# Kernel optimization log

Hardware: AMD Instinct MI355X
Metric: run time of the kernel (lower is better)

## Reference

```python
import jax, jax.numpy as jnp
import numpy as np

NW, NT, ND = 100000, 10000, 50000
D = 128
E = {"ww": 200000, "wt": 100000, "wd": 150000, "td": 100000, "tt": 50000}


def setup_inputs() -> dict:
    key = jax.random.key(0)
    ks = iter(jax.random.split(key, 40))
    inp = {
        "h_word": jax.random.normal(next(ks), (NW, D), dtype=jnp.float32),
        "h_topic": jax.random.normal(next(ks), (NT, D), dtype=jnp.float32),
        "h_doc": jax.random.normal(next(ks), (ND, D), dtype=jnp.float32),
    }
    for et in ["ww", "wt", "wd", "td", "tt"]:
        inp[f"W_{et}"] = jax.random.normal(next(ks), (D, D), dtype=jnp.float32) * 0.05
        inp[f"b_{et}"] = jax.random.normal(next(ks), (D,), dtype=jnp.float32) * 0.05
    sizes = {"ww": (NW, NW), "wt": (NW, NT), "wd": (NW, ND), "td": (NT, ND), "tt": (NT, NT)}
    for et, (ns, nd) in sizes.items():
        inp[f"src_{et}"] = jax.random.randint(next(ks), (E[et],), 0, ns, dtype=jnp.int32)
        inp[f"dst_{et}"] = jax.random.randint(next(ks), (E[et],), 0, nd, dtype=jnp.int32)
        inp[f"ew_{et}"] = jax.random.uniform(next(ks), (E[et],), dtype=jnp.float32)
    return inp


def _linear(x, W, b):
    # torch nn.Linear: y = x @ W.T + b, W is [out, in]
    return x @ W.T + b


def _mean_agg(h_src, src, dst, ew, n_dst):
    # message m_e = h_src[src_e] * ew_e (u_mul_e), then per-dst mean (fn.mean)
    m = h_src[src] * ew[:, None]                               # [E, D]
    s = jax.ops.segment_sum(m, dst, num_segments=n_dst)        # [n_dst, D]
    cnt = jax.ops.segment_sum(jnp.ones_like(ew), dst, num_segments=n_dst)
    return s / jnp.maximum(cnt, 1.0)[:, None]


def reference(h_word, h_topic, h_doc,
              W_ww, b_ww, W_wt, b_wt, W_wd, b_wd, W_td, b_td, W_tt, b_tt,
              src_ww, dst_ww, ew_ww, src_wt, dst_wt, ew_wt,
              src_wd, dst_wd, ew_wd, src_td, dst_td, ew_td,
              src_tt, dst_tt, ew_tt):
    # DGL loop overwrites src node 'h' in-place -> linears COMPOSE per src type,
    # and messages (resolved at multi_update_all) use the final composed 'h'.
    hw = _linear(_linear(_linear(h_word, W_ww, b_ww), W_wt, b_wt), W_wd, b_wd)
    ht = _linear(_linear(h_topic, W_td, b_td), W_tt, b_tt)
    nw, nt, nd = h_word.shape[0], h_topic.shape[0], h_doc.shape[0]
    # cross-relation 'sum' of per-relation means
    out_word = _mean_agg(hw, src_ww, dst_ww, ew_ww, nw)
    out_topic = _mean_agg(hw, src_wt, dst_wt, ew_wt, nt) + _mean_agg(ht, src_tt, dst_tt, ew_tt, nt)
    out_doc = _mean_agg(hw, src_wd, dst_wd, ew_wd, nd) + _mean_agg(ht, src_td, dst_td, ew_td, nd)
    # relu + dropout (eval mode -> identity); concatenate node types for a single output
    return jnp.concatenate([
        jax.nn.relu(out_word), jax.nn.relu(out_topic), jax.nn.relu(out_doc)
    ], axis=0)
```

## Files before the change

kernel.cpp:

```cpp
#include <hip/hip_runtime.h>
#include <hip/hip_bf16.h>

#define DIM 128
#define NWORD 100000
#define NTOPIC 10000
#define NDOC 50000
#define NOUT (NWORD + NTOPIC + NDOC)

#define E_WW 200000
#define E_WT 100000
#define E_WD 150000
#define E_TD 100000
#define E_TT 50000
#define E_TOT 600000

#define B_WW 0
#define B_WT 100000
#define B_TT 110000
#define B_WD 120000
#define B_TD 170000
#define NSLOT 220000
#define NBLK_SCAN 215

#define NBW 512
#define NBT 64

typedef __attribute__((ext_vector_type(8))) short bf16x8;
typedef __attribute__((ext_vector_type(8))) unsigned short u16x8;
typedef __attribute__((ext_vector_type(4))) float f32x4;

__device__ __forceinline__ unsigned short f2bf(float f) {
    __hip_bfloat16 h = __float2bfloat16(f);
    return __builtin_bit_cast(unsigned short, h);
}
__device__ __forceinline__ float b2f(unsigned short u) {
    return __builtin_bit_cast(float, (unsigned)u << 16);
}

__global__ __launch_bounds__(128) void prep1(
    const float* __restrict__ W_ww, const float* __restrict__ b_ww,
    const float* __restrict__ W_wt, const float* __restrict__ b_wt,
    const float* __restrict__ W_wd, const float* __restrict__ b_wd,
    const float* __restrict__ W_td, const float* __restrict__ b_td,
    const float* __restrict__ W_tt, const float* __restrict__ b_tt,
    float* __restrict__ A, unsigned short* __restrict__ Wbf_t,
    float* __restrict__ tmpb, float* __restrict__ c_t, unsigned* __restrict__ cnt)
{
    int b = blockIdx.x, j = threadIdx.x;
    for (int i = b * 128 + j; i < NSLOT; i += gridDim.x * 128) cnt[i] = 0u;

    if (b < 128) {
        const float* wr = &W_wd[b * 128];
        float s0 = 0.f, s1 = 0.f, s2 = 0.f, s3 = 0.f;
        for (int m = 0; m < 128; m += 4) {
            s0 = fmaf(wr[m + 0], W_wt[(m + 0) * 128 + j], s0);
            s1 = fmaf(wr[m + 1], W_wt[(m + 1) * 128 + j], s1);
            s2 = fmaf(wr[m + 2], W_wt[(m + 2) * 128 + j], s2);
            s3 = fmaf(wr[m + 3], W_wt[(m + 3) * 128 + j], s3);
        }
        A[b * 128 + j] = (s0 + s1) + (s2 + s3);
    } else if (b < 256) {
        int k = b - 128;
        const float* wr = &W_tt[j * 128];
        float s0 = 0.f, s1 = 0.f, s2 = 0.f, s3 = 0.f;
        for (int m = 0; m < 128; m += 4) {
            s0 = fmaf(wr[m + 0], W_td[(m + 0) * 128 + k], s0);
            s1 = fmaf(wr[m + 1], W_td[(m + 1) * 128 + k], s1);
            s2 = fmaf(wr[m + 2], W_td[(m + 2) * 128 + k], s2);
            s3 = fmaf(wr[m + 3], W_td[(m + 3) * 128 + k], s3);
        }
        Wbf_t[j * 128 + k] = f2bf((s0 + s1) + (s2 + s3));
    } else if (b == 256) {
        float s = b_wt[j];
        for (int m = 0; m < 128; ++m) s = fmaf(W_wt[j * 128 + m], b_ww[m], s);
        tmpb[j] = s;
    } else {
        float s = b_tt[j];
        for (int m = 0; m < 128; ++m) s = fmaf(W_tt[j * 128 + m], b_td[m], s);
        c_t[j] = s;
    }
}

__global__ __launch_bounds__(256) void prep2(
    const float* __restrict__ W_ww, const float* __restrict__ W_wd,
    const float* __restrict__ b_wd, const float* __restrict__ A,
    const float* __restrict__ tmpb,
    unsigned short* __restrict__ Wbf_w, float* __restrict__ c_w,
    const int* __restrict__ dst_ww, const int* __restrict__ dst_wt,
    const int* __restrict__ dst_wd, const int* __restrict__ dst_td,
    const int* __restrict__ dst_tt,
    unsigned* __restrict__ cnt, unsigned* __restrict__ rank)
{
    int b = blockIdx.x, tid = threadIdx.x;
    if (b < 64) {
        int k = b * 2 + (tid >> 7), j = tid & 127;
        const float* ar = &A[j * 128];
        float s0 = 0.f, s1 = 0.f, s2 = 0.f, s3 = 0.f;
        for (int m = 0; m < 128; m += 4) {
            s0 = fmaf(ar[m + 0], W_ww[(m + 0) * 128 + k], s0);
            s1 = fmaf(ar[m + 1], W_ww[(m + 1) * 128 + k], s1);
            s2 = fmaf(ar[m + 2], W_ww[(m + 2) * 128 + k], s2);
            s3 = fmaf(ar[m + 3], W_ww[(m + 3) * 128 + k], s3);
        }
        Wbf_w[j * 128 + k] = f2bf((s0 + s1) + (s2 + s3));
    } else if (b == 64) {
        if (tid < 128) {
            float s = b_wd[tid];
            for (int m = 0; m < 128; ++m) s = fmaf(W_wd[tid * 128 + m], tmpb[m], s);
            c_w[tid] = s;
        }
    } else {
        int g = (b - 65) * 256 + tid;
        int slotidx;
        if (g < E_WW)                            slotidx = B_WW + dst_ww[g];
        else if (g < E_WW + E_WT)                slotidx = B_WT + dst_wt[g - E_WW];
        else if (g < E_WW + E_WT + E_WD)         slotidx = B_WD + dst_wd[g - E_WW - E_WT];
        else if (g < E_WW + E_WT + E_WD + E_TD)  slotidx = B_TD + dst_td[g - E_WW - E_WT - E_WD];
        else if (g < E_TOT)                      slotidx = B_TT + dst_tt[g - E_WW - E_WT - E_WD - E_TD];
        else return;
        rank[g] = atomicAdd(&cnt[slotidx], 1u);
    }
}

__global__ __launch_bounds__(256) void transform_mfma(
    const float* __restrict__ xw, const unsigned short* __restrict__ Wbf_w,
    const float* __restrict__ cw, unsigned short* __restrict__ yw, int ntw,
    const float* __restrict__ xt, const unsigned short* __restrict__ Wbf_t,
    const float* __restrict__ ct, unsigned short* __restrict__ yt, int ntt)
{
    __shared__ __attribute__((aligned(16))) unsigned short xs_all[4][16 * 128];
    const int tid = threadIdx.x;
    const int wid = tid >> 6, l = tid & 63;
    char* xs = (char*)xs_all[wid];
    const int l15 = l & 15, l4 = l >> 4;

    const bool isw = blockIdx.x < NBW;
    const float* x = isw ? xw : xt;
    const unsigned short* Wbf = isw ? Wbf_w : Wbf_t;
    const float* bias = isw ? cw : ct;
    unsigned short* y = isw ? yw : yt;
    const int nt = isw ? ntw : ntt;
    const int t0 = (isw ? blockIdx.x : blockIdx.x - NBW) * 4 + wid;
    const int tstr = (isw ? NBW : NBT) * 4;

    bf16x8 wf[8][4];
#pragma unroll
    for (int cg = 0; cg < 8; ++cg)
#pragma unroll
        for (int ki = 0; ki < 4; ++ki)
            wf[cg][ki] = *(const bf16x8*)&Wbf[(cg * 16 + l15) * 128 + ki * 32 + l4 * 8];

    float bj[8];
#pragma unroll
    for (int cg = 0; cg < 8; ++cg) bj[cg] = bias[cg * 16 + l15];

    const int row_s = l >> 2, ch = l & 3;

    float4 u[4], v[4];
    if (t0 < nt) {
        const float* xr = &x[((size_t)t0 * 16 + row_s) * 128 + ch * 32];
#pragma unroll
        for (int c = 0; c < 4; ++c) { u[c] = *(const float4*)(xr + c * 8); v[c] = *(const float4*)(xr + c * 8 + 4); }
    }

    for (int tile = t0; tile < nt; tile += tstr) {
#pragma unroll
        for (int c = 0; c < 4; ++c) {
            u16x8 p;
            p[0] = f2bf(u[c].x); p[1] = f2bf(u[c].y); p[2] = f2bf(u[c].z); p[3] = f2bf(u[c].w);
            p[4] = f2bf(v[c].x); p[5] = f2bf(v[c].y); p[6] = f2bf(v[c].z); p[7] = f2bf(v[c].w);
            int off = row_s * 256 + ((ch * 64 + c * 16) ^ ((row_s & 7) << 4));
            *(u16x8*)(xs + off) = p;
        }
        int nxt = tile + tstr;
        if (nxt < nt) {
            const float* xr = &x[((size_t)nxt * 16 + row_s) * 128 + ch * 32];
#pragma unroll
            for (int c = 0; c < 4; ++c) { u[c] = *(const float4*)(xr + c * 8); v[c] = *(const float4*)(xr + c * 8 + 4); }
        }

        f32x4 acc[8];
        const f32x4 zero = {0.f, 0.f, 0.f, 0.f};
#pragma unroll
        for (int cg = 0; cg < 8; ++cg) acc[cg] = zero;

#pragma unroll
        for (int ki = 0; ki < 4; ++ki) {
            int aoff = l15 * 256 + ((ki * 64 + l4 * 16) ^ ((l15 & 7) << 4));
            bf16x8 af = *(const bf16x8*)(xs + aoff);
#pragma unroll
            for (int cg = 0; cg < 8; ++cg)
                acc[cg] = __builtin_amdgcn_mfma_f32_16x16x32_bf16(af, wf[cg][ki], acc[cg], 0, 0, 0);
        }

        unsigned short* yr = &y[((size_t)tile * 16 + l4 * 4) * 128 + l15];
#pragma unroll
        for (int cg = 0; cg < 8; ++cg)
#pragma unroll
            for (int r = 0; r < 4; ++r)
                yr[r * 128 + cg * 16] = f2bf(acc[cg][r] + bj[cg]);
    }
}

__global__ __launch_bounds__(256) void scanA(const unsigned* __restrict__ cnt,
                                             unsigned* __restrict__ bsum)
{
    __shared__ unsigned sh[256];
    int t = threadIdx.x;
    int base = blockIdx.x * 1024 + t * 4;
    unsigned s = 0;
#pragma unroll
    for (int i = 0; i < 4; ++i) { int idx = base + i; if (idx < NSLOT) s += cnt[idx]; }
    sh[t] = s; __syncthreads();
    for (int o = 128; o > 0; o >>= 1) { if (t < o) sh[t] += sh[t + o]; __syncthreads(); }
    if (t == 0) bsum[blockIdx.x] = sh[0];
}

__global__ __launch_bounds__(256) void scanB(const unsigned* __restrict__ bsum,
                                             unsigned* __restrict__ boff)
{
    __shared__ unsigned sh[256];
    int t = threadIdx.x;
    unsigned v = (t < NBLK_SCAN) ? bsum[t] : 0u;
    sh[t] = v; __syncthreads();
    for (int o = 1; o < 256; o <<= 1) {
        unsigned x = (t >= o) ? sh[t - o] : 0u;
        __syncthreads();
        sh[t] += x;
        __syncthreads();
    }
    if (t < NBLK_SCAN) boff[t] = sh[t] - v;
}

__global__ __launch_bounds__(256) void scanC(const unsigned* __restrict__ cnt,
                                             const unsigned* __restrict__ boff,
                                             unsigned* __restrict__ offs)
{
    __shared__ unsigned sh[256];
    int t = threadIdx.x;
    int base = blockIdx.x * 1024 + t * 4;
    unsigned c[4]; unsigned s = 0;
#pragma unroll
    for (int i = 0; i < 4; ++i) {
        int idx = base + i;
        c[i] = (idx < NSLOT) ? cnt[idx] : 0u;
        s += c[i];
    }
    sh[t] = s; __syncthreads();
    for (int o = 1; o < 256; o <<= 1) {
        unsigned x = (t >= o) ? sh[t - o] : 0u;
        __syncthreads();
        sh[t] += x;
        __syncthreads();
    }
    unsigned run = boff[blockIdx.x] + sh[t] - s;
#pragma unroll
    for (int i = 0; i < 4; ++i) {
        int idx = base + i;
        if (idx < NSLOT) {
            offs[idx] = run;
            run += c[i];
            if (idx == NSLOT - 1) offs[NSLOT] = run;
        }
    }
}

__global__ void place(const int* __restrict__ dst_ww, const int* __restrict__ dst_wt,
                      const int* __restrict__ dst_wd, const int* __restrict__ dst_td,
                      const int* __restrict__ dst_tt,
                      const int* __restrict__ src_ww, const int* __restrict__ src_wt,
                      const int* __restrict__ src_wd, const int* __restrict__ src_td,
                      const int* __restrict__ src_tt,
                      const float* __restrict__ ew_ww, const float* __restrict__ ew_wt,
                      const float* __restrict__ ew_wd, const float* __restrict__ ew_td,
                      const float* __restrict__ ew_tt,
                      const unsigned* __restrict__ offs, const unsigned* __restrict__ rank,
                      uint2* __restrict__ se)
{
    int g = blockIdx.x * 256 + threadIdx.x;
    int slotidx, e; unsigned sv; float wv;
    if (g < E_WW)                            { e = g;                             slotidx = B_WW + dst_ww[e]; sv = src_ww[e]; wv = ew_ww[e]; }
    else if (g < E_WW + E_WT)                { e = g - E_WW;                      slotidx = B_WT + dst_wt[e]; sv = src_wt[e]; wv = ew_wt[e]; }
    else if (g < E_WW + E_WT + E_WD)         { e = g - E_WW - E_WT;               slotidx = B_WD + dst_wd[e]; sv = src_wd[e]; wv = ew_wd[e]; }
    else if (g < E_WW + E_WT + E_WD + E_TD)  { e = g - E_WW - E_WT - E_WD;        slotidx = B_TD + dst_td[e]; sv = src_td[e]; wv = ew_td[e]; }
    else if (g < E_TOT)                      { e = g - E_WW - E_WT - E_WD - E_TD; slotidx = B_TT + dst_tt[e]; sv = src_tt[e]; wv = ew_tt[e]; }
    else return;
    se[offs[slotidx] + rank[g]] = make_uint2(sv, __builtin_bit_cast(unsigned, wv));
}

__device__ __forceinline__ float4 seg_mean_bf(int slot,
                                              const unsigned* __restrict__ offs,
                                              const uint2* __restrict__ se,
                                              const unsigned short* __restrict__ h, int d4)
{
    unsigned off = offs[slot];
    unsigned deg = offs[slot + 1] - off;
    float ax = 0.f, ay = 0.f, az = 0.f, aw = 0.f;
    for (unsigned j = 0; j < deg; j += 4) {
        uint2 r0 = se[off + j];
        uint2 r1 = se[off + j + 1];
        uint2 r2 = se[off + j + 2];
        uint2 r3 = se[off + j + 3];
        unsigned s0 = r0.x;
        float    w0 = __builtin_bit_cast(float, r0.y);
        unsigned s1 = (j + 1 < deg) ? r1.x : 0u;
        float    w1 = (j + 1 < deg) ? __builtin_bit_cast(float, r1.y) : 0.f;
        unsigned s2 = (j + 2 < deg) ? r2.x : 0u;
        float    w2 = (j + 2 < deg) ? __builtin_bit_cast(float, r2.y) : 0.f;
        unsigned s3 = (j + 3 < deg) ? r3.x : 0u;
        float    w3 = (j + 3 < deg) ? __builtin_bit_cast(float, r3.y) : 0.f;
        ushort4 a0 = *(const ushort4*)&h[(size_t)s0 * 128 + d4];
        ushort4 a1 = *(const ushort4*)&h[(size_t)s1 * 128 + d4];
        ushort4 a2 = *(const ushort4*)&h[(size_t)s2 * 128 + d4];
        ushort4 a3 = *(const ushort4*)&h[(size_t)s3 * 128 + d4];
        ax = fmaf(b2f(a0.x), w0, ax); ay = fmaf(b2f(a0.y), w0, ay);
        az = fmaf(b2f(a0.z), w0, az); aw = fmaf(b2f(a0.w), w0, aw);
        ax = fmaf(b2f(a1.x), w1, ax); ay = fmaf(b2f(a1.y), w1, ay);
        az = fmaf(b2f(a1.z), w1, az); aw = fmaf(b2f(a1.w), w1, aw);
        ax = fmaf(b2f(a2.x), w2, ax); ay = fmaf(b2f(a2.y), w2, ay);
        az = fmaf(b2f(a2.z), w2, az); aw = fmaf(b2f(a2.w), w2, aw);
        ax = fmaf(b2f(a3.x), w3, ax); ay = fmaf(b2f(a3.y), w3, ay);
        az = fmaf(b2f(a3.z), w3, az); aw = fmaf(b2f(a3.w), w3, aw);
    }
    float inv = 1.0f / (float)(deg > 1u ? deg : 1u);
    return float4{ax * inv, ay * inv, az * inv, aw * inv};
}

__global__ void gather(const unsigned* __restrict__ offs,
                       const uint2* __restrict__ se,
                       const unsigned short* __restrict__ hw,
                       const unsigned short* __restrict__ ht,
                       float* __restrict__ out)
{
    int g = blockIdx.x * 256 + threadIdx.x;
    int n = g >> 5, d4 = (g & 31) << 2;
    if (n >= NOUT) return;
    float4 r;
    if (n < NWORD) {
        r = seg_mean_bf(B_WW + n, offs, se, hw, d4);
    } else if (n < NWORD + NTOPIC) {
        int i = n - NWORD;
        float4 a = seg_mean_bf(B_WT + i, offs, se, hw, d4);
        float4 b = seg_mean_bf(B_TT + i, offs, se, ht, d4);
        r = float4{a.x + b.x, a.y + b.y, a.z + b.z, a.w + b.w};
    } else {
        int i = n - NWORD - NTOPIC;
        float4 a = seg_mean_bf(B_WD + i, offs, se, hw, d4);
        float4 b = seg_mean_bf(B_TD + i, offs, se, ht, d4);
        r = float4{a.x + b.x, a.y + b.y, a.z + b.z, a.w + b.w};
    }
    r.x = fmaxf(r.x, 0.f); r.y = fmaxf(r.y, 0.f);
    r.z = fmaxf(r.z, 0.f); r.w = fmaxf(r.w, 0.f);
    *reinterpret_cast<float4*>(&out[(size_t)n * 128 + d4]) = r;
}

extern "C" void kernel_launch(void* const* d_in, const int* in_sizes, int n_in,
                              void* d_out, int out_size, void* d_ws, size_t ws_size,
                              hipStream_t stream) {
    const float* h_word  = (const float*)d_in[0];
    const float* h_topic = (const float*)d_in[1];
    const float* W_ww = (const float*)d_in[3];  const float* b_ww = (const float*)d_in[4];
    const float* W_wt = (const float*)d_in[5];  const float* b_wt = (const float*)d_in[6];
    const float* W_wd = (const float*)d_in[7];  const float* b_wd = (const float*)d_in[8];
    const float* W_td = (const float*)d_in[9];  const float* b_td = (const float*)d_in[10];
    const float* W_tt = (const float*)d_in[11]; const float* b_tt = (const float*)d_in[12];
    const int*   src_ww = (const int*)d_in[13]; const int* dst_ww = (const int*)d_in[14];
    const float* ew_ww  = (const float*)d_in[15];
    const int*   src_wt = (const int*)d_in[16]; const int* dst_wt = (const int*)d_in[17];
    const float* ew_wt  = (const float*)d_in[18];
    const int*   src_wd = (const int*)d_in[19]; const int* dst_wd = (const int*)d_in[20];
    const float* ew_wd  = (const float*)d_in[21];
    const int*   src_td = (const int*)d_in[22]; const int* dst_td = (const int*)d_in[23];
    const float* ew_td  = (const float*)d_in[24];
    const int*   src_tt = (const int*)d_in[25]; const int* dst_tt = (const int*)d_in[26];
    const float* ew_tt  = (const float*)d_in[27];

    float* out = (float*)d_out;

    unsigned short* hw_bf = (unsigned short*)d_ws;
    unsigned short* ht_bf = hw_bf + (size_t)NWORD * 128;
    unsigned short* Wbf_w = ht_bf + (size_t)NTOPIC * 128;
    unsigned short* Wbf_t = Wbf_w + 16384;
    float* fbase = (float*)(Wbf_t + 16384);
    float* c_w   = fbase;
    float* c_t   = c_w + 128;
    float* Amat  = c_t + 128;
    float* tmpb  = Amat + 16384;
    uint2* se    = (uint2*)(tmpb + 128);
    unsigned* cnt  = (unsigned*)(se + E_TOT + 4);
    unsigned* offs = cnt + NSLOT;
    unsigned* rank = offs + NSLOT + 1;
    unsigned* bsum = rank + E_TOT;
    unsigned* boff = bsum + 256;

    prep1<<<258, 128, 0, stream>>>(W_ww, b_ww, W_wt, b_wt, W_wd, b_wd, W_td, b_td,
                                   W_tt, b_tt, Amat, Wbf_t, tmpb, c_t, cnt);
    prep2<<<65 + (E_TOT + 255) / 256, 256, 0, stream>>>(
        W_ww, W_wd, b_wd, Amat, tmpb, Wbf_w, c_w,
        dst_ww, dst_wt, dst_wd, dst_td, dst_tt, cnt, rank);

    scanA<<<NBLK_SCAN, 256, 0, stream>>>(cnt, bsum);
    scanB<<<1, 256, 0, stream>>>(bsum, boff);
    scanC<<<NBLK_SCAN, 256, 0, stream>>>(cnt, boff, offs);
    place<<<(E_TOT + 255) / 256, 256, 0, stream>>>(
        dst_ww, dst_wt, dst_wd, dst_td, dst_tt,
        src_ww, src_wt, src_wd, src_td, src_tt,
        ew_ww, ew_wt, ew_wd, ew_td, ew_tt, offs, rank, se);

    transform_mfma<<<NBW + NBT, 256, 0, stream>>>(
        h_word,  Wbf_w, c_w, hw_bf, NWORD / 16,
        h_topic, Wbf_t, c_t, ht_bf, NTOPIC / 16);

    gather<<<(NOUT * 32 + 255) / 256, 256, 0, stream>>>(offs, se, hw_bf, ht_bf, out);
}
```

Measured before the change: 301.3 us.

## Fuse CSR build into one persistent kernel with grid barriers; split gather across half-waves

Merges prep2, the three scan kernels and the place kernel into a single persistent csr_build kernel. It uses 215 co-resident blocks that synchronise through atomic grid barriers, which removes four kernel launches and their inter-kernel gaps. The gather kernel now gives each output node 64 lanes: word nodes split their edge loop across two halves, and topic and doc nodes handle their two relations in parallel halves, combined with a cross-lane shuffle. This adds parallelism per node. The transform block counts also change. The grid barrier depends on all blocks being resident at once, which risks deadlock if occupancy assumptions fail.

Measured after the change: 347.6 us. 1.15x slower.

```diff
diff --git a/kernel.cpp b/kernel.cpp
--- a/kernel.cpp
+++ b/kernel.cpp
@@ -20,10 +20,11 @@
 #define B_WD 120000
 #define B_TD 170000
 #define NSLOT 220000
-#define NBLK_SCAN 215
-
-#define NBW 512
-#define NBT 64
+
+#define NBLK_CSR 215
+
+#define NBW 466
+#define NBT 46
 
 typedef __attribute__((ext_vector_type(8))) short bf16x8;
 typedef __attribute__((ext_vector_type(8))) unsigned short u16x8;
@@ -35,6 +36,24 @@
 }
 __device__ __forceinline__ float b2f(unsigned short u) {
     return __builtin_bit_cast(float, (unsigned)u << 16);
+}
+
+#define AGENT __HIP_MEMORY_SCOPE_AGENT
+__device__ __forceinline__ unsigned aload(const unsigned* p) {
+    return __hip_atomic_load(p, __ATOMIC_RELAXED, AGENT);
+}
+__device__ __forceinline__ void astore(unsigned* p, unsigned v) {
+    __hip_atomic_store(p, v, __ATOMIC_RELAXED, AGENT);
+}
+
+__device__ __forceinline__ void gbar(unsigned* bar, unsigned target) {
+    __syncthreads();
+    if (threadIdx.x == 0) {
+        __hip_atomic_fetch_add(bar, 1u, __ATOMIC_ACQ_REL, AGENT);
+        while (__hip_atomic_load(bar, __ATOMIC_ACQUIRE, AGENT) < target)
+            __builtin_amdgcn_s_sleep(4);
+    }
+    __syncthreads();
 }
 
 __global__ __launch_bounds__(128) void prep1(
@@ -44,10 +63,10 @@
     const float* __restrict__ W_td, const float* __restrict__ b_td,
     const float* __restrict__ W_tt, const float* __restrict__ b_tt,
     float* __restrict__ A, unsigned short* __restrict__ Wbf_t,
-    float* __restrict__ tmpb, float* __restrict__ c_t, unsigned* __restrict__ cnt)
+    float* __restrict__ tmpb, float* __restrict__ c_t, unsigned* __restrict__ zbase)
 {
     int b = blockIdx.x, j = threadIdx.x;
-    for (int i = b * 128 + j; i < NSLOT; i += gridDim.x * 128) cnt[i] = 0u;
+    for (int i = b * 128 + j; i < NSLOT + 16; i += gridDim.x * 128) zbase[i] = 0u;
 
     if (b < 128) {
         const float* wr = &W_wd[b * 128];
@@ -81,7 +100,18 @@
     }
 }
 
-__global__ __launch_bounds__(256) void prep2(
+__device__ __forceinline__ int edge_slot(
+    int g, const int* __restrict__ dw, const int* __restrict__ dt,
+    const int* __restrict__ dd, const int* __restrict__ dtd, const int* __restrict__ dtt)
+{
+    if (g < E_WW)                           return B_WW + dw[g];
+    if (g < E_WW + E_WT)                    return B_WT + dt[g - E_WW];
+    if (g < E_WW + E_WT + E_WD)             return B_WD + dd[g - E_WW - E_WT];
+    if (g < E_WW + E_WT + E_WD + E_TD)      return B_TD + dtd[g - E_WW - E_WT - E_WD];
+    return B_TT + dtt[g - E_WW - E_WT - E_WD - E_TD];
+}
+
+__global__ __launch_bounds__(256) void csr_build(
     const float* __restrict__ W_ww, const float* __restrict__ W_wd,
     const float* __restrict__ b_wd, const float* __restrict__ A,
     const float* __restrict__ tmpb,
@@ -89,11 +119,21 @@
     const int* __restrict__ dst_ww, const int* __restrict__ dst_wt,
     const int* __restrict__ dst_wd, const int* __restrict__ dst_td,
     const int* __restrict__ dst_tt,
-    unsigned* __restrict__ cnt, unsigned* __restrict__ rank)
-{
-    int b = blockIdx.x, tid = threadIdx.x;
+    const int* __restrict__ src_ww, const int* __restrict__ src_wt,
+    const int* __restrict__ src_wd, const int* __restrict__ src_td,
+    const int* __restrict__ src_tt,
+    const float* __restrict__ ew_ww, const float* __restrict__ ew_wt,
+    const float* __restrict__ ew_wd, const float* __restrict__ ew_td,
+    const float* __restrict__ ew_tt,
+    unsigned* __restrict__ cnt, unsigned* __restrict__ rank,
+    unsigned* __restrict__ offs, unsigned* __restrict__ bsum,
+    unsigned* __restrict__ bar, uint2* __restrict__ se)
+{
+    __shared__ unsigned sh[256];
+    const int b = blockIdx.x, t = threadIdx.x;
+
     if (b < 64) {
-        int k = b * 2 + (tid >> 7), j = tid & 127;
+        int k = b * 2 + (t >> 7), j = t & 127;
         const float* ar = &A[j * 128];
         float s0 = 0.f, s1 = 0.f, s2 = 0.f, s3 = 0.f;
         for (int m = 0; m < 128; m += 4) {
@@ -103,22 +143,57 @@
             s3 = fmaf(ar[m + 3], W_ww[(m + 3) * 128 + k], s3);
         }
         Wbf_w[j * 128 + k] = f2bf((s0 + s1) + (s2 + s3));
-    } else if (b == 64) {
-        if (tid < 128) {
-            float s = b_wd[tid];
-            for (int m = 0; m < 128; ++m) s = fmaf(W_wd[tid * 128 + m], tmpb[m], s);
-            c_w[tid] = s;
-        }
-    } else {
-        int g = (b - 65) * 256 + tid;
-        int slotidx;
-        if (g < E_WW)                            slotidx = B_WW + dst_ww[g];
-        else if (g < E_WW + E_WT)                slotidx = B_WT + dst_wt[g - E_WW];
-        else if (g < E_WW + E_WT + E_WD)         slotidx = B_WD + dst_wd[g - E_WW - E_WT];
-        else if (g < E_WW + E_WT + E_WD + E_TD)  slotidx = B_TD + dst_td[g - E_WW - E_WT - E_WD];
-        else if (g < E_TOT)                      slotidx = B_TT + dst_tt[g - E_WW - E_WT - E_WD - E_TD];
-        else return;
-        rank[g] = atomicAdd(&cnt[slotidx], 1u);
+    } else if (b == 64 && t < 128) {
+        float s = b_wd[t];
+        for (int m = 0; m < 128; ++m) s = fmaf(W_wd[t * 128 + m], tmpb[m], s);
+        c_w[t] = s;
+    }
+    for (int g = b * 256 + t; g < E_TOT; g += NBLK_CSR * 256) {
+        int slotidx = edge_slot(g, dst_ww, dst_wt, dst_wd, dst_td, dst_tt);
+        unsigned r = atomicAdd(&cnt[slotidx], 1u);
+        astore(&rank[g], r);
+    }
+    gbar(bar, NBLK_CSR);
+
+    const int base = b * 1024 + t * 4;
+    unsigned c0 = 0, c1 = 0, c2 = 0, c3 = 0;
+    if (base + 0 < NSLOT) c0 = aload(&cnt[base + 0]);
+    if (base + 1 < NSLOT) c1 = aload(&cnt[base + 1]);
+    if (base + 2 < NSLOT) c2 = aload(&cnt[base + 2]);
+    if (base + 3 < NSLOT) c3 = aload(&cnt[base + 3]);
+    unsigned s = c0 + c1 + c2 + c3;
+    sh[t] = s; __syncthreads();
+    for (int o = 1; o < 256; o <<= 1) {
+        unsigned x = (t >= o) ? sh[t - o] : 0u;
+        __syncthreads();
+        sh[t] += x;
+        __syncthreads();
+    }
+    const unsigned excl = sh[t] - s;
+    if (t == 0) astore(&bsum[b], sh[255]);
+    gbar(bar, 2 * NBLK_CSR);
+
+    unsigned p = (t < b) ? aload(&bsum[t]) : 0u;
+    sh[t] = p; __syncthreads();
+    for (int o = 128; o > 0; o >>= 1) { if (t < o) sh[t] += sh[t + o]; __syncthreads(); }
+    unsigned run = sh[0] + excl;
+    if (base + 0 < NSLOT) { astore(&offs[base + 0], run); run += c0; }
+    if (base + 1 < NSLOT) { astore(&offs[base + 1], run); run += c1; }
+    if (base + 2 < NSLOT) { astore(&offs[base + 2], run); run += c2; }
+    if (base + 3 < NSLOT) { astore(&offs[base + 3], run); run += c3; }
+    if (b == 0 && t == 0) astore(&offs[NSLOT], (unsigned)E_TOT);
+    gbar(bar, 3 * NBLK_CSR);
+
+    for (int g = b * 256 + t; g < E_TOT; g += NBLK_CSR * 256) {
+        int slotidx, e; unsigned sv; float wv;
+        if (g < E_WW)                           { e = g;                             slotidx = B_WW + dst_ww[e]; sv = src_ww[e]; wv = ew_ww[e]; }
+        else if (g < E_WW + E_WT)               { e = g - E_WW;                      slotidx = B_WT + dst_wt[e]; sv = src_wt[e]; wv = ew_wt[e]; }
+        else if (g < E_WW + E_WT + E_WD)        { e = g - E_WW - E_WT;               slotidx = B_WD + dst_wd[e]; sv = src_wd[e]; wv = ew_wd[e]; }
+        else if (g < E_WW + E_WT + E_WD + E_TD) { e = g - E_WW - E_WT - E_WD;        slotidx = B_TD + dst_td[e]; sv = src_td[e]; wv = ew_td[e]; }
+        else                                    { e = g - E_WW - E_WT - E_WD - E_TD; slotidx = B_TT + dst_tt[e]; sv = src_tt[e]; wv = ew_tt[e]; }
+        unsigned r = aload(&rank[g]);
+        unsigned o = aload(&offs[slotidx]);
+        se[o + r] = make_uint2(sv, __builtin_bit_cast(unsigned, wv));
     }
 }
 
@@ -202,113 +277,25 @@
     }
 }
 
-__global__ __launch_bounds__(256) void scanA(const unsigned* __restrict__ cnt,
-                                             unsigned* __restrict__ bsum)
-{
-    __shared__ unsigned sh[256];
-    int t = threadIdx.x;
-    int base = blockIdx.x * 1024 + t * 4;
-    unsigned s = 0;
-#pragma unroll
-    for (int i = 0; i < 4; ++i) { int idx = base + i; if (idx < NSLOT) s += cnt[idx]; }
-    sh[t] = s; __syncthreads();
-    for (int o = 128; o > 0; o >>= 1) { if (t < o) sh[t] += sh[t + o]; __syncthreads(); }
-    if (t == 0) bsum[blockIdx.x] = sh[0];
-}
-
-__global__ __launch_bounds__(256) void scanB(const unsigned* __restrict__ bsum,
-                                             unsigned* __restrict__ boff)
-{
-    __shared__ unsigned sh[256];
-    int t = threadIdx.x;
-    unsigned v = (t < NBLK_SCAN) ? bsum[t] : 0u;
-    sh[t] = v; __syncthreads();
-    for (int o = 1; o < 256; o <<= 1) {
-        unsigned x = (t >= o) ? sh[t - o] : 0u;
-        __syncthreads();
-        sh[t] += x;
-        __syncthreads();
-    }
-    if (t < NBLK_SCAN) boff[t] = sh[t] - v;
-}
-
-__global__ __launch_bounds__(256) void scanC(const unsigned* __restrict__ cnt,
-                                             const unsigned* __restrict__ boff,
-                                             unsigned* __restrict__ offs)
-{
-    __shared__ unsigned sh[256];
-    int t = threadIdx.x;
-    int base = blockIdx.x * 1024 + t * 4;
-    unsigned c[4]; unsigned s = 0;
-#pragma unroll
-    for (int i = 0; i < 4; ++i) {
-        int idx = base + i;
-        c[i] = (idx < NSLOT) ? cnt[idx] : 0u;
-        s += c[i];
-    }
-    sh[t] = s; __syncthreads();
-    for (int o = 1; o < 256; o <<= 1) {
-        unsigned x = (t >= o) ? sh[t - o] : 0u;
-        __syncthreads();
-        sh[t] += x;
-        __syncthreads();
-    }
-    unsigned run = boff[blockIdx.x] + sh[t] - s;
-#pragma unroll
-    for (int i = 0; i < 4; ++i) {
-        int idx = base + i;
-        if (idx < NSLOT) {
-            offs[idx] = run;
-            run += c[i];
-            if (idx == NSLOT - 1) offs[NSLOT] = run;
-        }
-    }
-}
-
-__global__ void place(const int* __restrict__ dst_ww, const int* __restrict__ dst_wt,
-                      const int* __restrict__ dst_wd, const int* __restrict__ dst_td,
-                      const int* __restrict__ dst_tt,
-                      const int* __restrict__ src_ww, const int* __restrict__ src_wt,
-                      const int* __restrict__ src_wd, const int* __restrict__ src_td,
-                      const int* __restrict__ src_tt,
-                      const float* __restrict__ ew_ww, const float* __restrict__ ew_wt,
-                      const float* __restrict__ ew_wd, const float* __restrict__ ew_td,
-                      const float* __restrict__ ew_tt,
-                      const unsigned* __restrict__ offs, const unsigned* __restrict__ rank,
-                      uint2* __restrict__ se)
-{
-    int g = blockIdx.x * 256 + threadIdx.x;
-    int slotidx, e; unsigned sv; float wv;
-    if (g < E_WW)                            { e = g;                             slotidx = B_WW + dst_ww[e]; sv = src_ww[e]; wv = ew_ww[e]; }
-    else if (g < E_WW + E_WT)                { e = g - E_WW;                      slotidx = B_WT + dst_wt[e]; sv = src_wt[e]; wv = ew_wt[e]; }
-    else if (g < E_WW + E_WT + E_WD)         { e = g - E_WW - E_WT;               slotidx = B_WD + dst_wd[e]; sv = src_wd[e]; wv = ew_wd[e]; }
-    else if (g < E_WW + E_WT + E_WD + E_TD)  { e = g - E_WW - E_WT - E_WD;        slotidx = B_TD + dst_td[e]; sv = src_td[e]; wv = ew_td[e]; }
-    else if (g < E_TOT)                      { e = g - E_WW - E_WT - E_WD - E_TD; slotidx = B_TT + dst_tt[e]; sv = src_tt[e]; wv = ew_tt[e]; }
-    else return;
-    se[offs[slotidx] + rank[g]] = make_uint2(sv, __builtin_bit_cast(unsigned, wv));
-}
-
-__device__ __forceinline__ float4 seg_mean_bf(int slot,
-                                              const unsigned* __restrict__ offs,
-                                              const uint2* __restrict__ se,
-                                              const unsigned short* __restrict__ h, int d4)
-{
-    unsigned off = offs[slot];
-    unsigned deg = offs[slot + 1] - off;
+__device__ __forceinline__ float4 seg_sum4(unsigned off, unsigned deg, unsigned j0,
+                                           unsigned step,
+                                           const uint2* __restrict__ se,
+                                           const unsigned short* __restrict__ h, int d4)
+{
     float ax = 0.f, ay = 0.f, az = 0.f, aw = 0.f;
-    for (unsigned j = 0; j < deg; j += 4) {
+    for (unsigned j = j0; j < deg; j += 4 * step) {
         uint2 r0 = se[off + j];
-        uint2 r1 = se[off + j + 1];
-        uint2 r2 = se[off + j + 2];
-        uint2 r3 = se[off + j + 3];
+        uint2 r1 = se[off + j + step];
+        uint2 r2 = se[off + j + 2 * step];
+        uint2 r3 = se[off + j + 3 * step];
         unsigned s0 = r0.x;
         float    w0 = __builtin_bit_cast(float, r0.y);
-        unsigned s1 = (j + 1 < deg) ? r1.x : 0u;
-        float    w1 = (j + 1 < deg) ? __builtin_bit_cast(float, r1.y) : 0.f;
-        unsigned s2 = (j + 2 < deg) ? r2.x : 0u;
-        float    w2 = (j + 2 < deg) ? __builtin_bit_cast(float, r2.y) : 0.f;
-        unsigned s3 = (j + 3 < deg) ? r3.x : 0u;
-        float    w3 = (j + 3 < deg) ? __builtin_bit_cast(float, r3.y) : 0.f;
+        unsigned s1 = (j + step < deg) ? r1.x : 0u;
+        float    w1 = (j + step < deg) ? __builtin_bit_cast(float, r1.y) : 0.f;
+        unsigned s2 = (j + 2 * step < deg) ? r2.x : 0u;
+        float    w2 = (j + 2 * step < deg) ? __builtin_bit_cast(float, r2.y) : 0.f;
+        unsigned s3 = (j + 3 * step < deg) ? r3.x : 0u;
+        float    w3 = (j + 3 * step < deg) ? __builtin_bit_cast(float, r3.y) : 0.f;
         ushort4 a0 = *(const ushort4*)&h[(size_t)s0 * 128 + d4];
         ushort4 a1 = *(const ushort4*)&h[(size_t)s1 * 128 + d4];
         ushort4 a2 = *(const ushort4*)&h[(size_t)s2 * 128 + d4];
@@ -322,36 +309,51 @@
         ax = fmaf(b2f(a3.x), w3, ax); ay = fmaf(b2f(a3.y), w3, ay);
         az = fmaf(b2f(a3.z), w3, az); aw = fmaf(b2f(a3.w), w3, aw);
     }
-    float inv = 1.0f / (float)(deg > 1u ? deg : 1u);
-    return float4{ax * inv, ay * inv, az * inv, aw * inv};
-}
-
-__global__ void gather(const unsigned* __restrict__ offs,
-                       const uint2* __restrict__ se,
-                       const unsigned short* __restrict__ hw,
-                       const unsigned short* __restrict__ ht,
-                       float* __restrict__ out)
+    return float4{ax, ay, az, aw};
+}
+
+__global__ __launch_bounds__(256) void gather(
+    const unsigned* __restrict__ offs, const uint2* __restrict__ se,
+    const unsigned short* __restrict__ hw, const unsigned short* __restrict__ ht,
+    float* __restrict__ out)
 {
     int g = blockIdx.x * 256 + threadIdx.x;
-    int n = g >> 5, d4 = (g & 31) << 2;
+    int n = g >> 6;
+    int lane = g & 63;
+    int h = lane >> 5, d4 = (lane & 31) << 2;
     if (n >= NOUT) return;
     float4 r;
     if (n < NWORD) {
-        r = seg_mean_bf(B_WW + n, offs, se, hw, d4);
-    } else if (n < NWORD + NTOPIC) {
-        int i = n - NWORD;
-        float4 a = seg_mean_bf(B_WT + i, offs, se, hw, d4);
-        float4 b = seg_mean_bf(B_TT + i, offs, se, ht, d4);
-        r = float4{a.x + b.x, a.y + b.y, a.z + b.z, a.w + b.w};
+        unsigned off = offs[n], deg = offs[n + 1] - off;
+        float4 s = seg_sum4(off, deg, h, 2, se, hw, d4);
+        s.x += __shfl_xor(s.x, 32); s.y += __shfl_xor(s.y, 32);
+        s.z += __shfl_xor(s.z, 32); s.w += __shfl_xor(s.w, 32);
+        float inv = 1.0f / (float)(deg > 1u ? deg : 1u);
+        r = float4{s.x * inv, s.y * inv, s.z * inv, s.w * inv};
     } else {
-        int i = n - NWORD - NTOPIC;
-        float4 a = seg_mean_bf(B_WD + i, offs, se, hw, d4);
-        float4 b = seg_mean_bf(B_TD + i, offs, se, ht, d4);
-        r = float4{a.x + b.x, a.y + b.y, a.z + b.z, a.w + b.w};
-    }
-    r.x = fmaxf(r.x, 0.f); r.y = fmaxf(r.y, 0.f);
-    r.z = fmaxf(r.z, 0.f); r.w = fmaxf(r.w, 0.f);
-    *reinterpret_cast<float4*>(&out[(size_t)n * 128 + d4]) = r;
+        int slot; const unsigned short* hx;
+        if (n < NWORD + NTOPIC) {
+            int i = n - NWORD;
+            slot = (h == 0) ? (B_WT + i) : (B_TT + i);
+            hx = (h == 0) ? hw : ht;
+        } else {
+            int i = n - NWORD - NTOPIC;
+            slot = (h == 0) ? (B_WD + i) : (B_TD + i);
+            hx = (h == 0) ? hw : ht;
+        }
+        unsigned off = offs[slot], deg = offs[slot + 1] - off;
+        float4 s = seg_sum4(off, deg, 0, 1, se, hx, d4);
+        float inv = 1.0f / (float)(deg > 1u ? deg : 1u);
+        s.x *= inv; s.y *= inv; s.z *= inv; s.w *= inv;
+        s.x += __shfl_xor(s.x, 32); s.y += __shfl_xor(s.y, 32);
+        s.z += __shfl_xor(s.z, 32); s.w += __shfl_xor(s.w, 32);
+        r = s;
+    }
+    if (h == 0) {
+        r.x = fmaxf(r.x, 0.f); r.y = fmaxf(r.y, 0.f);
+        r.z = fmaxf(r.z, 0.f); r.w = fmaxf(r.w, 0.f);
+        *reinterpret_cast<float4*>(&out[(size_t)n * 128 + d4]) = r;
+    }
 }
 
 extern "C" void kernel_launch(void* const* d_in, const int* in_sizes, int n_in,
@@ -387,29 +389,25 @@
     float* Amat  = c_t + 128;
     float* tmpb  = Amat + 16384;
     uint2* se    = (uint2*)(tmpb + 128);
-    unsigned* cnt  = (unsigned*)(se + E_TOT + 4);
-    unsigned* offs = cnt + NSLOT;
+    unsigned* cnt  = (unsigned*)(se + E_TOT + 8);
+    unsigned* bar  = cnt + NSLOT;
+    unsigned* offs = bar + 16;
     unsigned* rank = offs + NSLOT + 1;
     unsigned* bsum = rank + E_TOT;
-    unsigned* boff = bsum + 256;
 
     prep1<<<258, 128, 0, stream>>>(W_ww, b_ww, W_wt, b_wt, W_wd, b_wd, W_td, b_td,
                                    W_tt, b_tt, Amat, Wbf_t, tmpb, c_t, cnt);
-    prep2<<<65 + (E_TOT + 255) / 256, 256, 0, stream>>>(
+
+    csr_build<<<NBLK_CSR, 256, 0, stream>>>(
         W_ww, W_wd, b_wd, Amat, tmpb, Wbf_w, c_w,
-        dst_ww, dst_wt, dst_wd, dst_td, dst_tt, cnt, rank);
-
-    scanA<<<NBLK_SCAN, 256, 0, stream>>>(cnt, bsum);
-    scanB<<<1, 256, 0, stream>>>(bsum, boff);
-    scanC<<<NBLK_SCAN, 256, 0, stream>>>(cnt, boff, offs);
-    place<<<(E_TOT + 255) / 256, 256, 0, stream>>>(
         dst_ww, dst_wt, dst_wd, dst_td, dst_tt,
         src_ww, src_wt, src_wd, src_td, src_tt,
-        ew_ww, ew_wt, ew_wd, ew_td, ew_tt, offs, rank, se);
+        ew_ww, ew_wt, ew_wd, ew_td, ew_tt,
+        cnt, rank, offs, bsum, bar, se);
 
     transform_mfma<<<NBW + NBT, 256, 0, stream>>>(
         h_word,  Wbf_w, c_w, hw_bf, NWORD / 16,
         h_topic, Wbf_t, c_t, ht_bf, NTOPIC / 16);
 
-    gather<<<(NOUT * 32 + 255) / 256, 256, 0, stream>>>(offs, se, hw_bf, ht_bf, out);
-}
+    gather<<<(NOUT * 64 + 255) / 256, 256, 0, stream>>>(offs, se, hw_bf, ht_bf, out);
+}
```
